# Optimization experiments

Hardware: AMD Instinct MI355X
Metric: run time of the kernel (lower is better)

## Reference

```python
import jax, jax.numpy as jnp
import numpy as np

B, S, C = 8192, 7, 30


def _iou(b1, b2):
    """Faithful replica of calculate_iou (including its intersect/area1 + area2 - intersect quirk).
    b1, b2: [..., 4] as (cx, cy, w, h). Returns [...] ."""
    area1 = b1[..., 2] * b1[..., 3]
    area2 = b2[..., 2] * b2[..., 3]
    max_left = jnp.maximum(b1[..., 0] - b1[..., 2] / 2, b2[..., 0] - b2[..., 2] / 2)
    min_right = jnp.minimum(b1[..., 0] + b1[..., 2] / 2, b2[..., 0] + b2[..., 2] / 2)
    max_top = jnp.maximum(b1[..., 1] - b1[..., 3] / 2, b2[..., 1] - b2[..., 3] / 2)
    min_bottom = jnp.minimum(b1[..., 1] + b1[..., 3] / 2, b2[..., 1] + b2[..., 3] / 2)
    inter = (min_right - max_left) * (min_bottom - max_top)
    overlap = (max_left < min_right) & (max_top < min_bottom)
    return jnp.where(overlap, inter / area1 + area2 - inter, 0.0)


def setup_inputs() -> dict:
    key = jax.random.key(0)
    k1, k2, k3 = jax.random.split(key, 3)
    preds = jax.random.uniform(k1, (B, S, S, C), dtype=jnp.float32, minval=0.01, maxval=1.0)
    labels = jax.random.uniform(k2, (B, S, S, C), dtype=jnp.float32, minval=0.01, maxval=1.0)
    obj = (jax.random.uniform(k3, (B, S, S)) < 0.3).astype(jnp.float32)
    labels = labels.at[..., 4].set(obj)  # objectness indicator in {0,1}
    return {"preds": preds, "labels": labels}


def reference(preds, labels):
    batch_size = labels.shape[0]
    obj = (labels[..., 4] == 1).astype(preds.dtype)  # [B,7,7]

    # IoUs are computed on detached values in the original (numpy round-trip)
    iou1 = jax.lax.stop_gradient(_iou(preds[..., 0:4], labels[..., 0:4]))
    iou2 = jax.lax.stop_gradient(_iou(preds[..., 5:9], labels[..., 5:9]))
    resp1 = iou1 > iou2  # box 1 responsible

    xy1 = jnp.sum((preds[..., 0:2] - labels[..., 0:2]) ** 2, axis=-1)
    xy2 = jnp.sum((preds[..., 5:7] - labels[..., 5:7]) ** 2, axis=-1)
    wh1 = jnp.sum((jnp.sqrt(preds[..., 2:4]) - jnp.sqrt(labels[..., 2:4])) ** 2, axis=-1)
    wh2 = jnp.sum((jnp.sqrt(preds[..., 7:9]) - jnp.sqrt(labels[..., 7:9])) ** 2, axis=-1)

    loss_xy = 5.0 * jnp.where(resp1, xy1, xy2)
    loss_wh = jnp.where(resp1, wh1, wh2)
    loss_obj = jnp.where(resp1, (preds[..., 4] - iou1) ** 2, (preds[..., 9] - iou2) ** 2)
    loss_noobj_objcell = 0.5 * jnp.where(resp1, (preds[..., 9] - iou2) ** 2, (preds[..., 4] - iou1) ** 2)
    loss_cls = jnp.sum((preds[..., 10:] - labels[..., 10:]) ** 2, axis=-1)

    obj_cell = loss_xy + loss_wh + loss_obj + loss_noobj_objcell + loss_cls
    noobj_cell = 0.5 * (preds[..., 4] ** 2 + preds[..., 9] ** 2)

    total = jnp.sum(obj * obj_cell + (1.0 - obj) * noobj_cell)
    return total / batch_size
```

## Files before the change

### kernel.cpp

```cpp
#include <hip/hip_runtime.h>

#define YB     8192
#define YS     7
#define YC     30
#define NCELLS (YB * YS * YS)
#define WCELLS 64
#define BLOCK  256
#define CPB    (4 * WCELLS)
#define NBLK   (NCELLS / CPB)
#define NPART  (NCELLS / WCELLS)

__device__ __forceinline__ float iou_quirk(float cx1, float cy1, float w1, float h1,
                                           float cx2, float cy2, float w2, float h2) {
    float area1 = w1 * h1;
    float area2 = w2 * h2;
    float max_left   = fmaxf(cx1 - w1 * 0.5f, cx2 - w2 * 0.5f);
    float min_right  = fminf(cx1 + w1 * 0.5f, cx2 + w2 * 0.5f);
    float max_top    = fmaxf(cy1 - h1 * 0.5f, cy2 - h2 * 0.5f);
    float min_bottom = fminf(cy1 + h1 * 0.5f, cy2 + h2 * 0.5f);
    float inter = (min_right - max_left) * (min_bottom - max_top);
    bool overlap = (max_left < min_right) && (max_top < min_bottom);
    return overlap ? (inter / area1 + area2 - inter) : 0.0f;
}

__global__ __launch_bounds__(BLOCK) void yolo_partial_kernel(const float* __restrict__ preds,
                                                             const float* __restrict__ labels,
                                                             float* __restrict__ partial) {
    __shared__ float lds[4][2][WCELLS * YC];

    const int tid  = threadIdx.x;
    const int lane = tid & 63;
    const int w    = tid >> 6;

    const long cell0 = (long)blockIdx.x * CPB + (long)w * WCELLS;
    const float4* gp = (const float4*)(preds  + cell0 * YC);
    const float4* gl = (const float4*)(labels + cell0 * YC);
    float* sp = &lds[w][0][0];
    float* sl = &lds[w][1][0];
    float4* sp4 = (float4*)sp;
    float4* sl4 = (float4*)sl;
    const int NV = WCELLS * YC / 4;

#if defined(__has_builtin) && __has_builtin(__builtin_amdgcn_global_load_lds)
    typedef const __attribute__((address_space(1))) void* as1_t;
    typedef __attribute__((address_space(3))) void* as3_t;
    for (int i = lane; i < NV; i += 64)
        __builtin_amdgcn_global_load_lds((as1_t)(gp + i), (as3_t)(sp4 + i), 16, 0, 0);
    for (int i = lane; i < NV; i += 64)
        __builtin_amdgcn_global_load_lds((as1_t)(gl + i), (as3_t)(sl4 + i), 16, 0, 0);
    asm volatile("s_waitcnt vmcnt(0)" ::: "memory");
    __builtin_amdgcn_sched_barrier(0);
#else
    for (int i = lane; i < NV; i += 64) sp4[i] = gp[i];
    for (int i = lane; i < NV; i += 64) sl4[i] = gl[i];
    asm volatile("s_waitcnt vmcnt(0) lgkmcnt(0)" ::: "memory");
    __builtin_amdgcn_sched_barrier(0);
#endif

    const float2* p2 = (const float2*)(sp + lane * YC);
    const float2* l2 = (const float2*)(sl + lane * YC);

    float pv[10], lv[10];
    #pragma unroll
    for (int i = 0; i < 5; ++i) {
        float2 a = p2[i]; pv[2 * i] = a.x; pv[2 * i + 1] = a.y;
        float2 b = l2[i]; lv[2 * i] = b.x; lv[2 * i + 1] = b.y;
    }
    float loss_cls = 0.0f;
    #pragma unroll
    for (int i = 5; i < 15; ++i) {
        float2 a = p2[i], b = l2[i];
        float dx = a.x - b.x, dy = a.y - b.y;
        loss_cls += dx * dx + dy * dy;
    }

    float iou1 = iou_quirk(pv[0], pv[1], pv[2], pv[3], lv[0], lv[1], lv[2], lv[3]);
    float iou2 = iou_quirk(pv[5], pv[6], pv[7], pv[8], lv[5], lv[6], lv[7], lv[8]);
    bool resp1 = iou1 > iou2;

    float dx1 = pv[0] - lv[0], dy1 = pv[1] - lv[1];
    float xy1 = dx1 * dx1 + dy1 * dy1;
    float dx2 = pv[5] - lv[5], dy2 = pv[6] - lv[6];
    float xy2 = dx2 * dx2 + dy2 * dy2;

    float sw1 = sqrtf(pv[2]) - sqrtf(lv[2]), sh1 = sqrtf(pv[3]) - sqrtf(lv[3]);
    float wh1 = sw1 * sw1 + sh1 * sh1;
    float sw2 = sqrtf(pv[7]) - sqrtf(lv[7]), sh2 = sqrtf(pv[8]) - sqrtf(lv[8]);
    float wh2 = sw2 * sw2 + sh2 * sh2;

    float d1 = pv[4] - iou1, d2 = pv[9] - iou2;
    float e1 = d1 * d1, e2 = d2 * d2;

    float loss_xy = 5.0f * (resp1 ? xy1 : xy2);
    float loss_wh = resp1 ? wh1 : wh2;
    float loss_obj = resp1 ? e1 : e2;
    float loss_noobj_objcell = 0.5f * (resp1 ? e2 : e1);

    float obj_cell = loss_xy + loss_wh + loss_obj + loss_noobj_objcell + loss_cls;
    float noobj_cell = 0.5f * (pv[4] * pv[4] + pv[9] * pv[9]);

    float v = (lv[4] == 1.0f) ? obj_cell : noobj_cell;

    for (int off = 32; off > 0; off >>= 1) v += __shfl_down(v, off);
    if (lane == 0) partial[blockIdx.x * 4 + w] = v;
}

__global__ __launch_bounds__(BLOCK) void yolo_final_kernel(const float* __restrict__ partial,
                                                           float* __restrict__ out) {
    __shared__ double w[BLOCK / 64];
    double s = 0.0;
    for (int i = threadIdx.x; i < NPART; i += BLOCK) s += (double)partial[i];
    for (int off = 32; off > 0; off >>= 1) s += __shfl_down(s, off);
    const int lane = threadIdx.x & 63, wid = threadIdx.x >> 6;
    if (lane == 0) w[wid] = s;
    __syncthreads();
    if (threadIdx.x == 0) out[0] = (float)((w[0] + w[1] + w[2] + w[3]) / (double)YB);
}

extern "C" void kernel_launch(void* const* d_in, const int* in_sizes, int n_in,
                              void* d_out, int out_size, void* d_ws, size_t ws_size,
                              hipStream_t stream) {
    const float* preds  = (const float*)d_in[0];
    const float* labels = (const float*)d_in[1];
    float* out = (float*)d_out;
    float* partial = (float*)d_ws;

    yolo_partial_kernel<<<NBLK, BLOCK, 0, stream>>>(preds, labels, partial);
    yolo_final_kernel<<<1, BLOCK, 0, stream>>>(partial, out);
}
```

Before: 28.91 us.

## Use persistent waves with double-buffered LDS staging of 32-cell tiles

Replaces the one-tile-per-wave launch with a fixed grid of 512 blocks whose waves loop over 32-cell tiles with a stride. The next tile is prefetched into a second LDS buffer with global_load_lds while the current one is computed, so load latency overlaps with compute. The final reduction now sums far fewer partials. The cost is that only half the lanes do compute per tile, and the loop adds per-tile waitcnt overhead.

```diff
diff --git a/kernel.cpp b/kernel.cpp
--- a/kernel.cpp
+++ b/kernel.cpp
@@ -1,14 +1,16 @@
 #include <hip/hip_runtime.h>
 
-#define YB     8192
-#define YS     7
-#define YC     30
-#define NCELLS (YB * YS * YS)
-#define WCELLS 64
-#define BLOCK  256
-#define CPB    (4 * WCELLS)
-#define NBLK   (NCELLS / CPB)
-#define NPART  (NCELLS / WCELLS)
+#define YB      8192
+#define YS      7
+#define YC      30
+#define NCELLS  (YB * YS * YS)
+#define TCELLS  32
+#define TBYTES  (TCELLS * YC * 4)
+#define TFLOATS (TCELLS * YC)
+#define NTILES  (NCELLS / TCELLS)
+#define BLOCK   256
+#define GRID    512
+#define NWAVES  (GRID * 4)
 
 __device__ __forceinline__ float iou_quirk(float cx1, float cy1, float w1, float h1,
                                            float cx2, float cy2, float w2, float h2) {
@@ -23,40 +25,9 @@
     return overlap ? (inter / area1 + area2 - inter) : 0.0f;
 }
 
-__global__ __launch_bounds__(BLOCK) void yolo_partial_kernel(const float* __restrict__ preds,
-                                                             const float* __restrict__ labels,
-                                                             float* __restrict__ partial) {
-    __shared__ float lds[4][2][WCELLS * YC];
-
-    const int tid  = threadIdx.x;
-    const int lane = tid & 63;
-    const int w    = tid >> 6;
-
-    const long cell0 = (long)blockIdx.x * CPB + (long)w * WCELLS;
-    const float4* gp = (const float4*)(preds  + cell0 * YC);
-    const float4* gl = (const float4*)(labels + cell0 * YC);
-    float* sp = &lds[w][0][0];
-    float* sl = &lds[w][1][0];
-    float4* sp4 = (float4*)sp;
-    float4* sl4 = (float4*)sl;
-    const int NV = WCELLS * YC / 4;
-
-#if defined(__has_builtin) && __has_builtin(__builtin_amdgcn_global_load_lds)
-    typedef const __attribute__((address_space(1))) void* as1_t;
-    typedef __attribute__((address_space(3))) void* as3_t;
-    for (int i = lane; i < NV; i += 64)
-        __builtin_amdgcn_global_load_lds((as1_t)(gp + i), (as3_t)(sp4 + i), 16, 0, 0);
-    for (int i = lane; i < NV; i += 64)
-        __builtin_amdgcn_global_load_lds((as1_t)(gl + i), (as3_t)(sl4 + i), 16, 0, 0);
-    asm volatile("s_waitcnt vmcnt(0)" ::: "memory");
-    __builtin_amdgcn_sched_barrier(0);
-#else
-    for (int i = lane; i < NV; i += 64) sp4[i] = gp[i];
-    for (int i = lane; i < NV; i += 64) sl4[i] = gl[i];
-    asm volatile("s_waitcnt vmcnt(0) lgkmcnt(0)" ::: "memory");
-    __builtin_amdgcn_sched_barrier(0);
-#endif
-
+__device__ __forceinline__ float cell_loss(const float* __restrict__ sp,
+                                           const float* __restrict__ sl, int lane) {
+    if (lane >= TCELLS) return 0.0f;
     const float2* p2 = (const float2*)(sp + lane * YC);
     const float2* l2 = (const float2*)(sl + lane * YC);
 
@@ -91,25 +62,98 @@
     float d1 = pv[4] - iou1, d2 = pv[9] - iou2;
     float e1 = d1 * d1, e2 = d2 * d2;
 
-    float loss_xy = 5.0f * (resp1 ? xy1 : xy2);
-    float loss_wh = resp1 ? wh1 : wh2;
-    float loss_obj = resp1 ? e1 : e2;
-    float loss_noobj_objcell = 0.5f * (resp1 ? e2 : e1);
-
-    float obj_cell = loss_xy + loss_wh + loss_obj + loss_noobj_objcell + loss_cls;
+    float obj_cell = 5.0f * (resp1 ? xy1 : xy2)
+                   + (resp1 ? wh1 : wh2)
+                   + (resp1 ? e1 : e2)
+                   + 0.5f * (resp1 ? e2 : e1)
+                   + loss_cls;
     float noobj_cell = 0.5f * (pv[4] * pv[4] + pv[9] * pv[9]);
 
-    float v = (lv[4] == 1.0f) ? obj_cell : noobj_cell;
+    return (lv[4] == 1.0f) ? obj_cell : noobj_cell;
+}
 
-    for (int off = 32; off > 0; off >>= 1) v += __shfl_down(v, off);
-    if (lane == 0) partial[blockIdx.x * 4 + w] = v;
+__global__ __launch_bounds__(BLOCK) void yolo_partial_kernel(const float* __restrict__ preds,
+                                                             const float* __restrict__ labels,
+                                                             float* __restrict__ partial) {
+    __shared__ float lds[4][2][2][TFLOATS];
+
+    const int tid  = threadIdx.x;
+    const int lane = tid & 63;
+    const int w    = tid >> 6;
+    const int wave_id = blockIdx.x * 4 + w;
+
+    float acc = 0.0f;
+
+#if defined(__has_builtin) && __has_builtin(__builtin_amdgcn_global_load_lds)
+    typedef const __attribute__((address_space(1))) char* g_t;
+    typedef __attribute__((address_space(3))) char* s_t;
+
+    #define STAGE_ARR(gbase, sbase)                                                        \
+        do {                                                                               \
+            __builtin_amdgcn_global_load_lds((g_t)((gbase) + lane * 16),                   \
+                                             (s_t)((sbase) + lane * 16), 16, 0, 0);        \
+            __builtin_amdgcn_global_load_lds((g_t)((gbase) + 1024 + lane * 16),            \
+                                             (s_t)((sbase) + 1024 + lane * 16), 16, 0, 0); \
+            __builtin_amdgcn_global_load_lds((g_t)((gbase) + 2048 + lane * 16),            \
+                                             (s_t)((sbase) + 2048 + lane * 16), 16, 0, 0); \
+            __builtin_amdgcn_global_load_lds((g_t)((gbase) + 3072 + lane * 4),             \
+                                             (s_t)((sbase) + 3072 + lane * 4), 4, 0, 0);   \
+            __builtin_amdgcn_global_load_lds((g_t)((gbase) + 3328 + lane * 4),             \
+                                             (s_t)((sbase) + 3328 + lane * 4), 4, 0, 0);   \
+            __builtin_amdgcn_global_load_lds((g_t)((gbase) + 3584 + lane * 4),             \
+                                             (s_t)((sbase) + 3584 + lane * 4), 4, 0, 0);   \
+        } while (0)
+
+    #define STAGE_TILE(tile, b)                                                            \
+        do {                                                                               \
+            const char* gp_ = (const char*)preds  + (size_t)(tile) * TBYTES;               \
+            const char* gl_ = (const char*)labels + (size_t)(tile) * TBYTES;               \
+            STAGE_ARR(gp_, (char*)&lds[w][(b)][0][0]);                                     \
+            STAGE_ARR(gl_, (char*)&lds[w][(b)][1][0]);                                     \
+        } while (0)
+
+    int t = wave_id;
+    int buf = 0;
+    STAGE_TILE(t, 0);
+
+    for (;;) {
+        const int tn = t + NWAVES;
+        if (tn >= NTILES) break;
+        STAGE_TILE(tn, buf ^ 1);
+        asm volatile("s_waitcnt vmcnt(12)" ::: "memory");
+        __builtin_amdgcn_sched_barrier(0);
+        acc += cell_loss(&lds[w][buf][0][0], &lds[w][buf][1][0], lane);
+        buf ^= 1;
+        t = tn;
+    }
+    asm volatile("s_waitcnt vmcnt(0)" ::: "memory");
+    __builtin_amdgcn_sched_barrier(0);
+    acc += cell_loss(&lds[w][buf][0][0], &lds[w][buf][1][0], lane);
+
+    #undef STAGE_TILE
+    #undef STAGE_ARR
+#else
+    for (int t = wave_id, buf = 0; t < NTILES; t += NWAVES, buf ^= 1) {
+        const float4* gp = (const float4*)((const char*)preds  + (size_t)t * TBYTES);
+        const float4* gl = (const float4*)((const char*)labels + (size_t)t * TBYTES);
+        float4* sp4 = (float4*)&lds[w][buf][0][0];
+        float4* sl4 = (float4*)&lds[w][buf][1][0];
+        for (int i = lane; i < TFLOATS / 4; i += 64) { sp4[i] = gp[i]; sl4[i] = gl[i]; }
+        asm volatile("s_waitcnt vmcnt(0) lgkmcnt(0)" ::: "memory");
+        __builtin_amdgcn_sched_barrier(0);
+        acc += cell_loss(&lds[w][buf][0][0], &lds[w][buf][1][0], lane);
+    }
+#endif
+
+    for (int off = 32; off > 0; off >>= 1) acc += __shfl_down(acc, off);
+    if (lane == 0) partial[wave_id] = acc;
 }
 
 __global__ __launch_bounds__(BLOCK) void yolo_final_kernel(const float* __restrict__ partial,
                                                            float* __restrict__ out) {
     __shared__ double w[BLOCK / 64];
     double s = 0.0;
-    for (int i = threadIdx.x; i < NPART; i += BLOCK) s += (double)partial[i];
+    for (int i = threadIdx.x; i < NWAVES; i += BLOCK) s += (double)partial[i];
     for (int off = 32; off > 0; off >>= 1) s += __shfl_down(s, off);
     const int lane = threadIdx.x & 63, wid = threadIdx.x >> 6;
     if (lane == 0) w[wid] = s;
@@ -125,6 +169,6 @@
     float* out = (float*)d_out;
     float* partial = (float*)d_ws;
 
-    yolo_partial_kernel<<<NBLK, BLOCK, 0, stream>>>(preds, labels, partial);
+    yolo_partial_kernel<<<GRID, BLOCK, 0, stream>>>(preds, labels, partial);
     yolo_final_kernel<<<1, BLOCK, 0, stream>>>(partial, out);
 }
```

New measurement: 25.27 us. 12.6% less time.
